# Optimization experiments

Hardware: AMD Instinct MI355X
Metric: run time of the kernel (lower is better)

## Reference

```python
import jax, jax.numpy as jnp
import numpy as np

THETA = 10000.0


def _apply_rope(xh, positions, theta):
    # xh: [B, H, S, d_k]; positions: [S] int
    d_k = xh.shape[-1]
    inv_freq = theta ** (-jnp.arange(0, d_k, 2, dtype=jnp.float32) / d_k)  # [d_k/2]
    angles = positions.astype(jnp.float32)[:, None] * inv_freq[None, :]     # [S, d_k/2]
    cos = jnp.cos(angles)
    sin = jnp.sin(angles)
    x1 = xh[..., 0::2]
    x2 = xh[..., 1::2]
    r1 = x1 * cos - x2 * sin
    r2 = x1 * sin + x2 * cos
    return jnp.stack([r1, r2], axis=-1).reshape(xh.shape)


def setup_inputs() -> dict:
    key = jax.random.key(0)
    ks = jax.random.split(key, 5)
    B, S, D = 2, 2048, 1024
    std = np.sqrt(1.0 / D).astype(np.float32)
    return {
        "x": jax.random.normal(ks[0], (B, S, D), dtype=jnp.float32),
        "token_positions": jnp.arange(S, dtype=jnp.int64 if jax.config.jax_enable_x64 else jnp.int32),
        "Wq": jax.random.normal(ks[1], (D, D), dtype=jnp.float32) * std,
        "Wk": jax.random.normal(ks[2], (D, D), dtype=jnp.float32) * std,
        "Wv": jax.random.normal(ks[3], (D, D), dtype=jnp.float32) * std,
        "Wo": jax.random.normal(ks[4], (D, D), dtype=jnp.float32) * std,
    }


def reference(x, token_positions, Wq, Wk, Wv, Wo):
    B, S, D = x.shape
    n_heads = 16
    d_k = D // n_heads

    # QKV projections (torch does x @ W.T)
    q = x @ Wq.T
    k = x @ Wk.T
    v = x @ Wv.T

    def split_heads(t):  # [B,S,D] -> [B,H,S,d_k]
        return t.reshape(B, S, n_heads, d_k).transpose(0, 2, 1, 3)

    qh = _apply_rope(split_heads(q), token_positions, THETA)
    kh = _apply_rope(split_heads(k), token_positions, THETA)
    vh = split_heads(v)

    scores = jnp.einsum("bhqd,bhkd->bhqk", qh, kh) / jnp.sqrt(jnp.float32(d_k))
    causal = jnp.tril(jnp.ones((S, S), dtype=bool))
    scores = jnp.where(causal, scores, -jnp.inf)
    attn = jax.nn.softmax(scores, axis=-1)

    out_h = jnp.einsum("bhqk,bhkd->bhqd", attn, vh)  # [B,H,S,d_k]
    out = out_h.transpose(0, 2, 1, 3).reshape(B, S, D)
    return out @ Wo.T
```

## Files before the change

kernel.cpp:

```cpp
#include <hip/hip_runtime.h>

typedef unsigned int u32;
typedef __attribute__((ext_vector_type(4))) short s16x4;
typedef __attribute__((ext_vector_type(8))) short short8;
typedef __attribute__((ext_vector_type(4))) float f32x4;

__device__ __forceinline__ unsigned short f2bf(float f) {
  union { float f; u32 u; } x; x.f = f;
  u32 u = x.u;
  return (unsigned short)((u + 0x7fffu + ((u >> 16) & 1u)) >> 16);
}
__device__ __forceinline__ float bf2f(unsigned short b) {
  union { u32 u; float f; } x; x.u = ((u32)b) << 16;
  return x.f;
}
__device__ __forceinline__ f32x4 mfma_bf16(short8 a, short8 b, f32x4 c) {
  return __builtin_amdgcn_mfma_f32_16x16x32_bf16(a, b, c, 0, 0, 0);
}
__device__ __forceinline__ f32x4 mfma16(s16x4 a, s16x4 b, f32x4 c) {
  return __builtin_amdgcn_mfma_f32_16x16x16bf16_1k(a, b, c, 0, 0, 0);
}

typedef __attribute__((address_space(3))) unsigned int lds_u32;
typedef const __attribute__((address_space(1))) unsigned int glb_u32;
__device__ __forceinline__ void gload_lds16(const unsigned short* g, unsigned short* l) {
  __builtin_amdgcn_global_load_lds((glb_u32*)g, (lds_u32*)l, 16, 0, 0);
}

__global__ __launch_bounds__(256) void cvt_all(const float* __restrict__ x,
                                               const float* __restrict__ wq,
                                               const float* __restrict__ wk,
                                               const float* __restrict__ wv,
                                               const float* __restrict__ wo,
                                               unsigned short* __restrict__ xb,
                                               unsigned short* __restrict__ wqkv,
                                               unsigned short* __restrict__ wob) {
  const int i = blockIdx.x * 256 + threadIdx.x;
  const float* src;
  unsigned short* dst;
  int off;
  if (i < (1 << 20)) {
    src = x; dst = xb; off = i;
  } else {
    const int j = i - (1 << 20);
    const int w = j >> 18;
    off = j & ((1 << 18) - 1);
    src = (w == 0) ? wq : (w == 1) ? wk : (w == 2) ? wv : wo;
    dst = (w == 3) ? wob : wqkv + ((size_t)w << 20);
  }
  float4 v = ((const float4*)src)[off];
  ushort4 o;
  o.x = f2bf(v.x); o.y = f2bf(v.y); o.z = f2bf(v.z); o.w = f2bf(v.w);
  ((ushort4*)dst)[off] = o;
}

__global__ __launch_bounds__(256) void gemm_qkv(const unsigned short* __restrict__ A,
                                                const unsigned short* __restrict__ B,
                                                unsigned short* __restrict__ qk,
                                                unsigned short* __restrict__ kk,
                                                unsigned short* __restrict__ vtm) {
  constexpr int K = 1024;
  __shared__ unsigned short As[2][128 * 32];
  __shared__ unsigned short Bs[2][128 * 32];
  const int tid = threadIdx.x;
  const int wave = tid >> 6, lane = tid & 63;
  const int l15 = lane & 15, quad = lane >> 4;
  const int wr = wave >> 1, wc = wave & 1;
  const int m0 = blockIdx.y * 128, n0 = blockIdx.x * 128;
  f32x4 acc[4][4] = {};
  const int srow = (lane >> 2), scol = (lane & 3) * 8;
  const unsigned short* Ag[2][2];
  const unsigned short* Bg[2][2];
#pragma unroll
  for (int s = 0; s < 2; ++s)
#pragma unroll
    for (int r = 0; r < 2; ++r) {
      Ag[s][r] = A + (size_t)(m0 + wave * 32 + r * 16 + srow) * K + s * 32 + scol;
      Bg[s][r] = B + (size_t)(n0 + wave * 32 + r * 16 + srow) * K + s * 32 + scol;
    }
  for (int k0 = 0; k0 < K; k0 += 64) {
    __syncthreads();
#pragma unroll
    for (int s = 0; s < 2; ++s)
#pragma unroll
      for (int r = 0; r < 2; ++r) {
        gload_lds16(Ag[s][r] + k0, &As[s][(wave * 32 + r * 16) * 32]);
        gload_lds16(Bg[s][r] + k0, &Bs[s][(wave * 32 + r * 16) * 32]);
      }
    __syncthreads();
#pragma unroll
    for (int s = 0; s < 2; ++s) {
      short8 a[4], b[4];
#pragma unroll
      for (int i = 0; i < 4; ++i) a[i] = *(const short8*)&As[s][(wr * 64 + i * 16 + l15) * 32 + quad * 8];
#pragma unroll
      for (int j = 0; j < 4; ++j) b[j] = *(const short8*)&Bs[s][(wc * 64 + j * 16 + l15) * 32 + quad * 8];
#pragma unroll
      for (int i = 0; i < 4; ++i)
#pragma unroll
        for (int j = 0; j < 4; ++j) acc[i][j] = mfma_bf16(a[i], b[j], acc[i][j]);
    }
  }
  const int proj = n0 >> 10;
  const int nn0 = (n0 & 1023) + wc * 64;
  if (proj < 2) {
    unsigned short* dst = (proj == 0) ? qk : kk;
#pragma unroll
    for (int i = 0; i < 4; ++i) {
      const int mb = m0 + wr * 64 + i * 16 + quad * 4;
#pragma unroll
      for (int j = 0; j < 4; ++j) {
        const int nn = nn0 + j * 16 + l15;
#pragma unroll
        for (int r = 0; r < 4; ++r) dst[(size_t)(mb + r) * 1024 + nn] = f2bf(acc[i][j][r]);
      }
    }
  } else {
#pragma unroll
    for (int i = 0; i < 4; ++i) {
      const int mb = m0 + wr * 64 + i * 16 + quad * 4;
      const int bb = mb >> 11, s = mb & 2047;
#pragma unroll
      for (int j = 0; j < 4; ++j) {
        const int nn = nn0 + j * 16 + l15;
        const int h = nn >> 6, d = nn & 63;
        ushort4 v4;
        v4.x = f2bf(acc[i][j][0]); v4.y = f2bf(acc[i][j][1]);
        v4.z = f2bf(acc[i][j][2]); v4.w = f2bf(acc[i][j][3]);
        *(ushort4*)&vtm[(((size_t)bb * 16 + h) * 64 + d) * 2048 + s] = v4;
      }
    }
  }
}

__global__ __launch_bounds__(256) void rope_kernel(unsigned short* __restrict__ q,
                                                   unsigned short* __restrict__ k,
                                                   const int* __restrict__ pos) {
  const int idx = blockIdx.x * 256 + threadIdx.x;
  const int i = idx & 31;
  const int h = (idx >> 5) & 15;
  const int s = (idx >> 9) & 2047;
  const int b = idx >> 20;
  const float p = (float)pos[s];
  const float inv = exp2f(-0.4152410118609203f * (float)i);
  float sn, cs;
  sincosf(p * inv, &sn, &cs);
  const float SC = 0.18033688011112042f;
  const float csq = cs * SC, snq = sn * SC;
  const size_t base = ((size_t)(b * 2048 + s)) * 1024 + h * 64 + 2 * i;
  {
    u32* qp = (u32*)(q + base);
    u32 w = *qp;
    float x1 = bf2f((unsigned short)(w & 0xffff)), x2 = bf2f((unsigned short)(w >> 16));
    *qp = (u32)f2bf(x1 * csq - x2 * snq) | ((u32)f2bf(x1 * snq + x2 * csq) << 16);
  }
  {
    u32* kp = (u32*)(k + base);
    u32 w = *kp;
    float x1 = bf2f((unsigned short)(w & 0xffff)), x2 = bf2f((unsigned short)(w >> 16));
    *kp = (u32)f2bf(x1 * cs - x2 * sn) | ((u32)f2bf(x1 * sn + x2 * cs) << 16);
  }
}

__global__ __launch_bounds__(64) void attn_kernel(const unsigned short* __restrict__ qk,
                                                  const unsigned short* __restrict__ kk,
                                                  const unsigned short* __restrict__ vtm,
                                                  unsigned short* __restrict__ om) {
  const int lane = threadIdx.x;
  const int l15 = lane & 15, quad = lane >> 4;
  const int bid = blockIdx.x;
  const int bh = bid & 31;
  const int qi = 63 - (bid >> 5);
  const int b = bh >> 4, h = bh & 15;
  const int qrow0 = qi << 5;
  const unsigned short* Qp = qk + (size_t)b * 2048 * 1024 + h * 64;
  const unsigned short* Krow = kk + (size_t)b * 2048 * 1024 + h * 64 + (size_t)l15 * 1024 + quad * 8;
  const unsigned short* Vrow = vtm + (size_t)bh * 64 * 2048 + (size_t)l15 * 2048 + quad * 4;
  short8 qf[2][2];
#pragma unroll
  for (int f = 0; f < 2; ++f)
#pragma unroll
    for (int hh = 0; hh < 2; ++hh)
      qf[f][hh] = *(const short8*)(Qp + (size_t)(qrow0 + f * 16 + l15) * 1024 + hh * 32 + quad * 8);
  f32x4 o4[2][4] = {};
  f32x4 ls[2] = {};
  s16x4 ones4;
#pragma unroll
  for (int j = 0; j < 4; ++j) ones4[j] = (short)0x3F80;
  const int nk = (qrow0 >> 6) + 1;
  short8 kb[4][2];
#pragma unroll
  for (int nt = 0; nt < 4; ++nt)
#pragma unroll
    for (int hh = 0; hh < 2; ++hh)
      kb[nt][hh] = *(const short8*)(Krow + (size_t)(nt * 16) * 1024 + hh * 32);
  for (int kt = 0; kt < nk; ++kt) {
    const int kbase = kt << 6;
    const bool needmask = (kbase + 63 > qrow0);
    s16x4 vb[4][4];
#pragma unroll
    for (int t = 0; t < 4; ++t)
#pragma unroll
      for (int nt = 0; nt < 4; ++nt)
        vb[t][nt] = *(const s16x4*)(Vrow + (size_t)t * 16 * 2048 + kbase + nt * 16);
    s16x4 p4[2][4];
    {
      f32x4 st[4];
#pragma unroll
      for (int nt = 0; nt < 4; ++nt) {
        f32x4 z = {};
        z = mfma_bf16(kb[nt][0], qf[0][0], z);
        z = mfma_bf16(kb[nt][1], qf[0][1], z);
        st[nt] = z;
      }
      const int qrow = qrow0 + l15;
#pragma unroll
      for (int nt = 0; nt < 4; ++nt) {
        f32x4 e;
#pragma unroll
        for (int r = 0; r < 4; ++r) e[r] = __builtin_amdgcn_exp2f(st[nt][r]);
        if (needmask) {
          const int kx = kbase + nt * 16 + quad * 4;
#pragma unroll
          for (int r = 0; r < 4; ++r)
            if (kx + r > qrow) e[r] = 0.f;
        }
        union { u32 u[2]; s16x4 s; } pk;
        pk.u[0] = __builtin_amdgcn_perm(__float_as_uint(e[1]), __float_as_uint(e[0]), 0x07060302u);
        pk.u[1] = __builtin_amdgcn_perm(__float_as_uint(e[3]), __float_as_uint(e[2]), 0x07060302u);
        p4[0][nt] = pk.s;
      }
    }
    {
      f32x4 st[4];
#pragma unroll
      for (int nt = 0; nt < 4; ++nt) {
        f32x4 z = {};
        z = mfma_bf16(kb[nt][0], qf[1][0], z);
        z = mfma_bf16(kb[nt][1], qf[1][1], z);
        st[nt] = z;
      }
      if (kt + 1 < nk) {
#pragma unroll
        for (int nt = 0; nt < 4; ++nt)
#pragma unroll
          for (int hh = 0; hh < 2; ++hh)
            kb[nt][hh] = *(const short8*)(Krow + (size_t)(kbase + 64 + nt * 16) * 1024 + hh * 32);
      }
      const int qrow = qrow0 + 16 + l15;
#pragma unroll
      for (int nt = 0; nt < 4; ++nt) {
        f32x4 e;
#pragma unroll
        for (int r = 0; r < 4; ++r) e[r] = __builtin_amdgcn_exp2f(st[nt][r]);
        if (needmask) {
          const int kx = kbase + nt * 16 + quad * 4;
#pragma unroll
          for (int r = 0; r < 4; ++r)
            if (kx + r > qrow) e[r] = 0.f;
        }
        union { u32 u[2]; s16x4 s; } pk;
        pk.u[0] = __builtin_amdgcn_perm(__float_as_uint(e[1]), __float_as_uint(e[0]), 0x07060302u);
        pk.u[1] = __builtin_amdgcn_perm(__float_as_uint(e[3]), __float_as_uint(e[2]), 0x07060302u);
        p4[1][nt] = pk.s;
      }
    }
#pragma unroll
    for (int nt = 0; nt < 4; ++nt) {
      ls[0] = mfma16(ones4, p4[0][nt], ls[0]);
      ls[1] = mfma16(ones4, p4[1][nt], ls[1]);
#pragma unroll
      for (int t = 0; t < 4; ++t) {
        o4[0][t] = mfma16(vb[t][nt], p4[0][nt], o4[0][t]);
        o4[1][t] = mfma16(vb[t][nt], p4[1][nt], o4[1][t]);
      }
    }
  }
#pragma unroll
  for (int f = 0; f < 2; ++f) {
    const int srow = qrow0 + f * 16 + l15;
    const float rl = 1.f / ls[f][0];
    unsigned short* orow = om + ((size_t)b * 2048 + srow) * 1024 + h * 64 + quad * 4;
#pragma unroll
    for (int t = 0; t < 4; ++t) {
      ushort4 o;
      o.x = f2bf(o4[f][t][0] * rl);
      o.y = f2bf(o4[f][t][1] * rl);
      o.z = f2bf(o4[f][t][2] * rl);
      o.w = f2bf(o4[f][t][3] * rl);
      *(ushort4*)(orow + t * 16) = o;
    }
  }
}

__global__ __launch_bounds__(256) void gemm_out(const unsigned short* __restrict__ A,
                                                const unsigned short* __restrict__ B,
                                                float* __restrict__ C) {
  constexpr int K = 1024;
  __shared__ unsigned short As[2][64 * 32];
  __shared__ unsigned short Bs[2][128 * 32];
  const int tid = threadIdx.x;
  const int wave = tid >> 6, lane = tid & 63;
  const int l15 = lane & 15, quad = lane >> 4;
  const int m0 = blockIdx.y * 64, n0 = blockIdx.x * 128;
  f32x4 acc[4][2] = {};
  const int srow = lane >> 2, scol = (lane & 3) * 8;
  const unsigned short* Ag[2];
  const unsigned short* Bg[2][2];
#pragma unroll
  for (int s = 0; s < 2; ++s) {
    Ag[s] = A + (size_t)(m0 + wave * 16 + srow) * K + s * 32 + scol;
#pragma unroll
    for (int r = 0; r < 2; ++r)
      Bg[s][r] = B + (size_t)(n0 + wave * 32 + r * 16 + srow) * K + s * 32 + scol;
  }
  for (int k0 = 0; k0 < K; k0 += 64) {
    __syncthreads();
#pragma unroll
    for (int s = 0; s < 2; ++s) {
      gload_lds16(Ag[s] + k0, &As[s][(wave * 16) * 32]);
#pragma unroll
      for (int r = 0; r < 2; ++r)
        gload_lds16(Bg[s][r] + k0, &Bs[s][(wave * 32 + r * 16) * 32]);
    }
    __syncthreads();
#pragma unroll
    for (int s = 0; s < 2; ++s) {
      short8 a[4], b[2];
#pragma unroll
      for (int i = 0; i < 4; ++i) a[i] = *(const short8*)&As[s][(i * 16 + l15) * 32 + quad * 8];
#pragma unroll
      for (int j = 0; j < 2; ++j) b[j] = *(const short8*)&Bs[s][(wave * 32 + j * 16 + l15) * 32 + quad * 8];
#pragma unroll
      for (int i = 0; i < 4; ++i)
#pragma unroll
        for (int j = 0; j < 2; ++j) acc[i][j] = mfma_bf16(a[i], b[j], acc[i][j]);
    }
  }
#pragma unroll
  for (int i = 0; i < 4; ++i)
#pragma unroll
    for (int j = 0; j < 2; ++j)
#pragma unroll
      for (int r = 0; r < 4; ++r)
        C[(size_t)(m0 + i * 16 + quad * 4 + r) * 1024 + n0 + wave * 32 + j * 16 + l15] =
            acc[i][j][r];
}

extern "C" void kernel_launch(void* const* d_in, const int* in_sizes, int n_in,
                              void* d_out, int out_size, void* d_ws, size_t ws_size,
                              hipStream_t stream) {
  const float* x  = (const float*)d_in[0];
  const int* pos  = (const int*)d_in[1];
  const float* Wq = (const float*)d_in[2];
  const float* Wk = (const float*)d_in[3];
  const float* Wv = (const float*)d_in[4];
  const float* Wo = (const float*)d_in[5];
  float* out = (float*)d_out;
  char* ws = (char*)d_ws;
  unsigned short* xb   = (unsigned short*)(ws);
  unsigned short* wqkv = (unsigned short*)(ws + (size_t)( 8 << 20));
  unsigned short* wob  = (unsigned short*)(ws + (size_t)(14 << 20));
  unsigned short* qkb  = (unsigned short*)(ws + (size_t)(16 << 20));
  unsigned short* kkb  = (unsigned short*)(ws + (size_t)(24 << 20));
  unsigned short* vtm  = (unsigned short*)(ws + (size_t)(32 << 20));
  unsigned short* om   = (unsigned short*)(ws + (size_t)(40 << 20));

  hipLaunchKernelGGL(cvt_all, dim3(8192), dim3(256), 0, stream, x, Wq, Wk, Wv, Wo, xb, wqkv, wob);
  hipLaunchKernelGGL(gemm_qkv, dim3(24, 32), dim3(256), 0, stream, xb, wqkv, qkb, kkb, vtm);
  hipLaunchKernelGGL(rope_kernel, dim3(8192), dim3(256), 0, stream, qkb, kkb, pos);
  hipLaunchKernelGGL(attn_kernel, dim3(2048), dim3(64), 0, stream, qkb, kkb, vtm, om);
  hipLaunchKernelGGL(gemm_out, dim3(8, 64), dim3(256), 0, stream, om, wob, out);
}
```

Baseline: 252.3 us.

## Fuse RoPE into QKV GEMM, head-major Q/K, split attention keys across waves

RoPE moves into the QKV GEMM epilogue. Q and K now use swapped MFMA operands so each lane holds adjacent column pairs, and they are written in a head-major layout, which removes the separate rope kernel and its read-modify-write pass. The attention kernel goes from 1 to 4 waves per block: each wave handles a strided subset of key tiles, and partial outputs and row sums are reduced through LDS. The output GEMM also swaps MFMA operands so it can store f32x4 vectors. Trade-offs are fast __sinf/__cosf with manual range reduction, which may lose accuracy, plus LDS reduction overhead and the loss of the K prefetch.

```diff
diff --git a/kernel.cpp b/kernel.cpp
--- a/kernel.cpp
+++ b/kernel.cpp
@@ -9,10 +9,6 @@
   union { float f; u32 u; } x; x.f = f;
   u32 u = x.u;
   return (unsigned short)((u + 0x7fffu + ((u >> 16) & 1u)) >> 16);
-}
-__device__ __forceinline__ float bf2f(unsigned short b) {
-  union { u32 u; float f; } x; x.u = ((u32)b) << 16;
-  return x.f;
 }
 __device__ __forceinline__ f32x4 mfma_bf16(short8 a, short8 b, f32x4 c) {
   return __builtin_amdgcn_mfma_f32_16x16x32_bf16(a, b, c, 0, 0, 0);
@@ -56,8 +52,9 @@
 
 __global__ __launch_bounds__(256) void gemm_qkv(const unsigned short* __restrict__ A,
                                                 const unsigned short* __restrict__ B,
-                                                unsigned short* __restrict__ qk,
-                                                unsigned short* __restrict__ kk,
+                                                const int* __restrict__ pos,
+                                                unsigned short* __restrict__ qhm,
+                                                unsigned short* __restrict__ khm,
                                                 unsigned short* __restrict__ vtm) {
   constexpr int K = 1024;
   __shared__ unsigned short As[2][128 * 32];
@@ -67,6 +64,7 @@
   const int l15 = lane & 15, quad = lane >> 4;
   const int wr = wave >> 1, wc = wave & 1;
   const int m0 = blockIdx.y * 128, n0 = blockIdx.x * 128;
+  const int proj = n0 >> 10;
   f32x4 acc[4][4] = {};
   const int srow = (lane >> 2), scol = (lane & 3) * 8;
   const unsigned short* Ag[2][2];
@@ -95,24 +93,57 @@
       for (int i = 0; i < 4; ++i) a[i] = *(const short8*)&As[s][(wr * 64 + i * 16 + l15) * 32 + quad * 8];
 #pragma unroll
       for (int j = 0; j < 4; ++j) b[j] = *(const short8*)&Bs[s][(wc * 64 + j * 16 + l15) * 32 + quad * 8];
-#pragma unroll
-      for (int i = 0; i < 4; ++i)
-#pragma unroll
-        for (int j = 0; j < 4; ++j) acc[i][j] = mfma_bf16(a[i], b[j], acc[i][j]);
-    }
-  }
-  const int proj = n0 >> 10;
+      if (proj < 2) {
+#pragma unroll
+        for (int i = 0; i < 4; ++i)
+#pragma unroll
+          for (int j = 0; j < 4; ++j) acc[i][j] = mfma_bf16(b[j], a[i], acc[i][j]);
+      } else {
+#pragma unroll
+        for (int i = 0; i < 4; ++i)
+#pragma unroll
+          for (int j = 0; j < 4; ++j) acc[i][j] = mfma_bf16(a[i], b[j], acc[i][j]);
+      }
+    }
+  }
   const int nn0 = (n0 & 1023) + wc * 64;
   if (proj < 2) {
-    unsigned short* dst = (proj == 0) ? qk : kk;
+    const int h = nn0 >> 6;
+    unsigned short* dst = ((proj == 0) ? qhm : khm);
+    const float SC = 0.18033688011112042f;
+    float cs[4][2], sn[4][2];
+#pragma unroll
+    for (int j = 0; j < 4; ++j) {
+      const int i0 = (j * 16 + quad * 4) >> 1;
+      cs[j][0] = exp2f(-0.4152410118609203f * (float)i0) * 0.15915494309189535f;
+      cs[j][1] = exp2f(-0.4152410118609203f * (float)(i0 + 1)) * 0.15915494309189535f;
+    }
 #pragma unroll
     for (int i = 0; i < 4; ++i) {
-      const int mb = m0 + wr * 64 + i * 16 + quad * 4;
+      const int m = m0 + wr * 64 + i * 16 + l15;
+      const int bb = m >> 11, ss = m & 2047;
+      const float p = (float)pos[ss];
+      unsigned short* base = dst + (((size_t)bb * 16 + h) * 2048 + ss) * 64;
 #pragma unroll
       for (int j = 0; j < 4; ++j) {
-        const int nn = nn0 + j * 16 + l15;
-#pragma unroll
-        for (int r = 0; r < 4; ++r) dst[(size_t)(mb + r) * 1024 + nn] = f2bf(acc[i][j][r]);
+        float c0, s0, c1, s1;
+        {
+          float rv = p * cs[j][0];
+          float ang = (rv - floorf(rv)) * 6.283185307179586f;
+          c0 = __cosf(ang); s0 = __sinf(ang);
+          rv = p * cs[j][1];
+          ang = (rv - floorf(rv)) * 6.283185307179586f;
+          c1 = __cosf(ang); s1 = __sinf(ang);
+        }
+        if (proj == 0) { c0 *= SC; s0 *= SC; c1 *= SC; s1 *= SC; }
+        const float x1 = acc[i][j][0], x2 = acc[i][j][1];
+        const float y1 = acc[i][j][2], y2 = acc[i][j][3];
+        ushort4 o;
+        o.x = f2bf(x1 * c0 - x2 * s0);
+        o.y = f2bf(x1 * s0 + x2 * c0);
+        o.z = f2bf(y1 * c1 - y2 * s1);
+        o.w = f2bf(y1 * s1 + y2 * c1);
+        *(ushort4*)(base + j * 16 + quad * 4) = o;
       }
     }
   } else {
@@ -133,70 +164,43 @@
   }
 }
 
-__global__ __launch_bounds__(256) void rope_kernel(unsigned short* __restrict__ q,
-                                                   unsigned short* __restrict__ k,
-                                                   const int* __restrict__ pos) {
-  const int idx = blockIdx.x * 256 + threadIdx.x;
-  const int i = idx & 31;
-  const int h = (idx >> 5) & 15;
-  const int s = (idx >> 9) & 2047;
-  const int b = idx >> 20;
-  const float p = (float)pos[s];
-  const float inv = exp2f(-0.4152410118609203f * (float)i);
-  float sn, cs;
-  sincosf(p * inv, &sn, &cs);
-  const float SC = 0.18033688011112042f;
-  const float csq = cs * SC, snq = sn * SC;
-  const size_t base = ((size_t)(b * 2048 + s)) * 1024 + h * 64 + 2 * i;
-  {
-    u32* qp = (u32*)(q + base);
-    u32 w = *qp;
-    float x1 = bf2f((unsigned short)(w & 0xffff)), x2 = bf2f((unsigned short)(w >> 16));
-    *qp = (u32)f2bf(x1 * csq - x2 * snq) | ((u32)f2bf(x1 * snq + x2 * csq) << 16);
-  }
-  {
-    u32* kp = (u32*)(k + base);
-    u32 w = *kp;
-    float x1 = bf2f((unsigned short)(w & 0xffff)), x2 = bf2f((unsigned short)(w >> 16));
-    *kp = (u32)f2bf(x1 * cs - x2 * sn) | ((u32)f2bf(x1 * sn + x2 * cs) << 16);
-  }
-}
-
-__global__ __launch_bounds__(64) void attn_kernel(const unsigned short* __restrict__ qk,
-                                                  const unsigned short* __restrict__ kk,
-                                                  const unsigned short* __restrict__ vtm,
-                                                  unsigned short* __restrict__ om) {
-  const int lane = threadIdx.x;
+__global__ __launch_bounds__(256) void attn_kernel(const unsigned short* __restrict__ qhm,
+                                                   const unsigned short* __restrict__ khm,
+                                                   const unsigned short* __restrict__ vtm,
+                                                   unsigned short* __restrict__ om) {
+  __shared__ float red[3][64][36];
+  const int tid = threadIdx.x;
+  const int wave = tid >> 6, lane = tid & 63;
   const int l15 = lane & 15, quad = lane >> 4;
   const int bid = blockIdx.x;
   const int bh = bid & 31;
   const int qi = 63 - (bid >> 5);
   const int b = bh >> 4, h = bh & 15;
   const int qrow0 = qi << 5;
-  const unsigned short* Qp = qk + (size_t)b * 2048 * 1024 + h * 64;
-  const unsigned short* Krow = kk + (size_t)b * 2048 * 1024 + h * 64 + (size_t)l15 * 1024 + quad * 8;
+  const unsigned short* Qp = qhm + (size_t)bh * 2048 * 64;
+  const unsigned short* Krow = khm + (size_t)bh * 2048 * 64 + (size_t)l15 * 64 + quad * 8;
   const unsigned short* Vrow = vtm + (size_t)bh * 64 * 2048 + (size_t)l15 * 2048 + quad * 4;
   short8 qf[2][2];
 #pragma unroll
   for (int f = 0; f < 2; ++f)
 #pragma unroll
     for (int hh = 0; hh < 2; ++hh)
-      qf[f][hh] = *(const short8*)(Qp + (size_t)(qrow0 + f * 16 + l15) * 1024 + hh * 32 + quad * 8);
+      qf[f][hh] = *(const short8*)(Qp + (size_t)(qrow0 + f * 16 + l15) * 64 + hh * 32 + quad * 8);
   f32x4 o4[2][4] = {};
   f32x4 ls[2] = {};
   s16x4 ones4;
 #pragma unroll
   for (int j = 0; j < 4; ++j) ones4[j] = (short)0x3F80;
   const int nk = (qrow0 >> 6) + 1;
-  short8 kb[4][2];
-#pragma unroll
-  for (int nt = 0; nt < 4; ++nt)
-#pragma unroll
-    for (int hh = 0; hh < 2; ++hh)
-      kb[nt][hh] = *(const short8*)(Krow + (size_t)(nt * 16) * 1024 + hh * 32);
-  for (int kt = 0; kt < nk; ++kt) {
+  for (int kt = wave; kt < nk; kt += 4) {
     const int kbase = kt << 6;
     const bool needmask = (kbase + 63 > qrow0);
+    short8 kb[4][2];
+#pragma unroll
+    for (int nt = 0; nt < 4; ++nt)
+#pragma unroll
+      for (int hh = 0; hh < 2; ++hh)
+        kb[nt][hh] = *(const short8*)(Krow + (size_t)(kbase + nt * 16) * 64 + hh * 32);
     s16x4 vb[4][4];
 #pragma unroll
     for (int t = 0; t < 4; ++t)
@@ -204,16 +208,17 @@
       for (int nt = 0; nt < 4; ++nt)
         vb[t][nt] = *(const s16x4*)(Vrow + (size_t)t * 16 * 2048 + kbase + nt * 16);
     s16x4 p4[2][4];
-    {
+#pragma unroll
+    for (int f = 0; f < 2; ++f) {
       f32x4 st[4];
 #pragma unroll
       for (int nt = 0; nt < 4; ++nt) {
         f32x4 z = {};
-        z = mfma_bf16(kb[nt][0], qf[0][0], z);
-        z = mfma_bf16(kb[nt][1], qf[0][1], z);
+        z = mfma_bf16(kb[nt][0], qf[f][0], z);
+        z = mfma_bf16(kb[nt][1], qf[f][1], z);
         st[nt] = z;
       }
-      const int qrow = qrow0 + l15;
+      const int qrow = qrow0 + f * 16 + l15;
 #pragma unroll
       for (int nt = 0; nt < 4; ++nt) {
         f32x4 e;
@@ -228,41 +233,7 @@
         union { u32 u[2]; s16x4 s; } pk;
         pk.u[0] = __builtin_amdgcn_perm(__float_as_uint(e[1]), __float_as_uint(e[0]), 0x07060302u);
         pk.u[1] = __builtin_amdgcn_perm(__float_as_uint(e[3]), __float_as_uint(e[2]), 0x07060302u);
-        p4[0][nt] = pk.s;
-      }
-    }
-    {
-      f32x4 st[4];
-#pragma unroll
-      for (int nt = 0; nt < 4; ++nt) {
-        f32x4 z = {};
-        z = mfma_bf16(kb[nt][0], qf[1][0], z);
-        z = mfma_bf16(kb[nt][1], qf[1][1], z);
-        st[nt] = z;
-      }
-      if (kt + 1 < nk) {
-#pragma unroll
-        for (int nt = 0; nt < 4; ++nt)
-#pragma unroll
-          for (int hh = 0; hh < 2; ++hh)
-            kb[nt][hh] = *(const short8*)(Krow + (size_t)(kbase + 64 + nt * 16) * 1024 + hh * 32);
-      }
-      const int qrow = qrow0 + 16 + l15;
-#pragma unroll
-      for (int nt = 0; nt < 4; ++nt) {
-        f32x4 e;
-#pragma unroll
-        for (int r = 0; r < 4; ++r) e[r] = __builtin_amdgcn_exp2f(st[nt][r]);
-        if (needmask) {
-          const int kx = kbase + nt * 16 + quad * 4;
-#pragma unroll
-          for (int r = 0; r < 4; ++r)
-            if (kx + r > qrow) e[r] = 0.f;
-        }
-        union { u32 u[2]; s16x4 s; } pk;
-        pk.u[0] = __builtin_amdgcn_perm(__float_as_uint(e[1]), __float_as_uint(e[0]), 0x07060302u);
-        pk.u[1] = __builtin_amdgcn_perm(__float_as_uint(e[3]), __float_as_uint(e[2]), 0x07060302u);
-        p4[1][nt] = pk.s;
+        p4[f][nt] = pk.s;
       }
     }
 #pragma unroll
@@ -276,19 +247,43 @@
       }
     }
   }
-#pragma unroll
-  for (int f = 0; f < 2; ++f) {
-    const int srow = qrow0 + f * 16 + l15;
-    const float rl = 1.f / ls[f][0];
-    unsigned short* orow = om + ((size_t)b * 2048 + srow) * 1024 + h * 64 + quad * 4;
-#pragma unroll
-    for (int t = 0; t < 4; ++t) {
-      ushort4 o;
-      o.x = f2bf(o4[f][t][0] * rl);
-      o.y = f2bf(o4[f][t][1] * rl);
-      o.z = f2bf(o4[f][t][2] * rl);
-      o.w = f2bf(o4[f][t][3] * rl);
-      *(ushort4*)(orow + t * 16) = o;
+  if (wave > 0) {
+    float* dst = &red[wave - 1][lane][0];
+#pragma unroll
+    for (int f = 0; f < 2; ++f)
+#pragma unroll
+      for (int t = 0; t < 4; ++t)
+        *(f32x4*)(dst + (f * 4 + t) * 4) = o4[f][t];
+    dst[32] = ls[0][0];
+    dst[33] = ls[1][0];
+  }
+  __syncthreads();
+  if (wave == 0) {
+#pragma unroll
+    for (int w = 0; w < 3; ++w) {
+      const float* s = &red[w][lane][0];
+#pragma unroll
+      for (int f = 0; f < 2; ++f)
+#pragma unroll
+        for (int t = 0; t < 4; ++t)
+          o4[f][t] += *(const f32x4*)(s + (f * 4 + t) * 4);
+      ls[0][0] += s[32];
+      ls[1][0] += s[33];
+    }
+#pragma unroll
+    for (int f = 0; f < 2; ++f) {
+      const int srow = qrow0 + f * 16 + l15;
+      const float rl = 1.f / ls[f][0];
+      unsigned short* orow = om + ((size_t)b * 2048 + srow) * 1024 + h * 64 + quad * 4;
+#pragma unroll
+      for (int t = 0; t < 4; ++t) {
+        ushort4 o;
+        o.x = f2bf(o4[f][t][0] * rl);
+        o.y = f2bf(o4[f][t][1] * rl);
+        o.z = f2bf(o4[f][t][2] * rl);
+        o.w = f2bf(o4[f][t][3] * rl);
+        *(ushort4*)(orow + t * 16) = o;
+      }
     }
   }
 }
@@ -334,17 +329,16 @@
 #pragma unroll
       for (int i = 0; i < 4; ++i)
 #pragma unroll
-        for (int j = 0; j < 2; ++j) acc[i][j] = mfma_bf16(a[i], b[j], acc[i][j]);
-    }
-  }
-#pragma unroll
-  for (int i = 0; i < 4; ++i)
+        for (int j = 0; j < 2; ++j) acc[i][j] = mfma_bf16(b[j], a[i], acc[i][j]);
+    }
+  }
+#pragma unroll
+  for (int i = 0; i < 4; ++i) {
+    float* row = C + (size_t)(m0 + i * 16 + l15) * 1024 + n0 + wave * 32 + quad * 4;
 #pragma unroll
     for (int j = 0; j < 2; ++j)
-#pragma unroll
-      for (int r = 0; r < 4; ++r)
-        C[(size_t)(m0 + i * 16 + quad * 4 + r) * 1024 + n0 + wave * 32 + j * 16 + l15] =
-            acc[i][j][r];
+      *(f32x4*)(row + j * 16) = acc[i][j];
+  }
 }
 
 extern "C" void kernel_launch(void* const* d_in, const int* in_sizes, int n_in,
@@ -361,14 +355,13 @@
   unsigned short* xb   = (unsigned short*)(ws);
   unsigned short* wqkv = (unsigned short*)(ws + (size_t)( 8 << 20));
   unsigned short* wob  = (unsigned short*)(ws + (size_t)(14 << 20));
-  unsigned short* qkb  = (unsigned short*)(ws + (size_t)(16 << 20));
-  unsigned short* kkb  = (unsigned short*)(ws + (size_t)(24 << 20));
+  unsigned short* qhm  = (unsigned short*)(ws + (size_t)(16 << 20));
+  unsigned short* khm  = (unsigned short*)(ws + (size_t)(24 << 20));
   unsigned short* vtm  = (unsigned short*)(ws + (size_t)(32 << 20));
   unsigned short* om   = (unsigned short*)(ws + (size_t)(40 << 20));
 
   hipLaunchKernelGGL(cvt_all, dim3(8192), dim3(256), 0, stream, x, Wq, Wk, Wv, Wo, xb, wqkv, wob);
-  hipLaunchKernelGGL(gemm_qkv, dim3(24, 32), dim3(256), 0, stream, xb, wqkv, qkb, kkb, vtm);
-  hipLaunchKernelGGL(rope_kernel, dim3(8192), dim3(256), 0, stream, qkb, kkb, pos);
-  hipLaunchKernelGGL(attn_kernel, dim3(2048), dim3(64), 0, stream, qkb, kkb, vtm, om);
+  hipLaunchKernelGGL(gemm_qkv, dim3(24, 32), dim3(256), 0, stream, xb, wqkv, pos, qhm, khm, vtm);
+  hipLaunchKernelGGL(attn_kernel, dim3(2048), dim3(256), 0, stream, qhm, khm, vtm, om);
   hipLaunchKernelGGL(gemm_out, dim3(8, 64), dim3(256), 0, stream, om, wob, out);
 }
```

Result: faster. 240.9 us (-4.5%).
